# Optimization experiments

Hardware: AMD Instinct MI355X
Metric: run time of the kernel (lower is better)

## Reference

```python
import jax, jax.numpy as jnp
import numpy as np

H_Q, H_KV, D_HEAD = 32, 4, 128

def setup_inputs() -> dict:
    key = jax.random.key(0)
    ks = jax.random.split(key, 5)
    B, S, H = 1, 4096, 2048
    hidden_states = jax.random.normal(ks[0], (B, S, H), jnp.float32)
    Wq = jax.random.normal(ks[1], (H, H_Q * D_HEAD), jnp.float32) * 0.02
    Wk = jax.random.normal(ks[2], (H, H_KV * D_HEAD), jnp.float32) * 0.02
    Wv = jax.random.normal(ks[3], (H, H_KV * D_HEAD), jnp.float32) * 0.02
    Wo = jax.random.normal(ks[4], (H_Q * D_HEAD, H), jnp.float32) * 0.02
    position_ids = jnp.arange(S, dtype=jnp.int32)
    # causal boolean mask, used as-is by the layer when rank != 2
    attention_mask = jnp.tril(jnp.ones((S, S), dtype=bool))[None, None]
    return dict(hidden_states=hidden_states, Wq=Wq, Wk=Wk, Wv=Wv, Wo=Wo,
                position_ids=position_ids, attention_mask=attention_mask)

def _rope(x, positions):
    # x: [B, S, H, D]; rotate-half style RoPE, max_wavelength=10000, scaling=1
    d = x.shape[-1]
    inv_freq = 1.0 / (10000.0 ** (jnp.arange(0, d, 2, dtype=jnp.float32) / d))  # [d/2]
    freq = positions.astype(jnp.float32)[:, None] * inv_freq[None, :]           # [S, d/2]
    emb = jnp.concatenate([freq, freq], axis=-1)                                # [S, d]
    cos = jnp.cos(emb)[None, :, None, :]
    sin = jnp.sin(emb)[None, :, None, :]
    x1, x2 = jnp.split(x, 2, axis=-1)
    rot = jnp.concatenate([-x2, x1], axis=-1)
    return x * cos + rot * sin

def reference(hidden_states, Wq, Wk, Wv, Wo, position_ids, attention_mask):
    B, S, H = hidden_states.shape
    q = (hidden_states @ Wq).reshape(B, S, H_Q, D_HEAD)
    k = (hidden_states @ Wk).reshape(B, S, H_KV, D_HEAD)
    v = (hidden_states @ Wv).reshape(B, S, H_KV, D_HEAD)
    q = _rope(q, position_ids)
    k = _rope(k, position_ids)
    q = q.transpose(0, 2, 1, 3)                                   # [B,Hq,S,D]
    num_groups = H_Q // H_KV
    k = jnp.repeat(k.transpose(0, 2, 1, 3), num_groups, axis=1)   # [B,Hq,S,D]
    v = jnp.repeat(v.transpose(0, 2, 1, 3), num_groups, axis=1)
    scores = jnp.einsum('bhqd,bhkd->bhqk', q, k) / jnp.sqrt(jnp.float32(D_HEAD))
    scores = jnp.where(attention_mask, scores, jnp.float32(-1e9))
    weights = jax.nn.softmax(scores, axis=-1)
    out = jnp.einsum('bhqk,bhkd->bhqd', weights, v)
    out = out.transpose(0, 2, 1, 3).reshape(B, S, H_Q * D_HEAD)
    return out @ Wo
```

## Files before the change

kernel.cpp:

```cpp
#include <hip/hip_runtime.h>
#include <hip/hip_bf16.h>

typedef __attribute__((ext_vector_type(8))) short bf16x8;
typedef __attribute__((ext_vector_type(4))) float f32x4;
typedef __attribute__((ext_vector_type(16))) float f32x16;

#define WAIT_VMCNT(n) asm volatile("s_waitcnt vmcnt(" #n ")" ::: "memory")
#define WAIT_LGKM0()  asm volatile("s_waitcnt lgkmcnt(0)" ::: "memory")

__device__ __forceinline__ unsigned short f2b(float f) {
  __hip_bfloat16 h = __float2bfloat16(f);
  return __builtin_bit_cast(unsigned short, h);
}
__device__ __forceinline__ float b2f(unsigned short u) {
  return __bfloat162float(__builtin_bit_cast(__hip_bfloat16, u));
}
__device__ __forceinline__ unsigned int pk2(float a, float b) {
  unsigned int r;
  asm("v_cvt_pk_bf16_f32 %0, %1, %2" : "=v"(r) : "v"(a), "v"(b));
  return r;
}

__device__ __forceinline__ void gld_lds16(const void* g, void* l) {
  __builtin_amdgcn_global_load_lds(
      (const __attribute__((address_space(1))) unsigned int*)g,
      (__attribute__((address_space(3))) unsigned int*)l, 16, 0, 0);
}

__global__ void convert_kernel(const float* __restrict__ in, unsigned short* __restrict__ out, int n4) {
  int i = blockIdx.x * blockDim.x + threadIdx.x;
  if (i >= n4) return;
  float4 v = ((const float4*)in)[i];
  uint2 o;
  o.x = pk2(v.x, v.y);
  o.y = pk2(v.z, v.w);
  *(uint2*)(out + (size_t)i * 4) = o;
}

__global__ void transpose_convert_kernel(const float* __restrict__ in, unsigned short* __restrict__ out,
                                         int R, int C) {
  __shared__ float tile[32][33];
  int c0 = blockIdx.x * 32, r0 = blockIdx.y * 32;
  int tx = threadIdx.x, ty = threadIdx.y;
#pragma unroll
  for (int k = 0; k < 32; k += 8)
    tile[ty + k][tx] = in[(size_t)(r0 + ty + k) * C + (c0 + tx)];
  __syncthreads();
#pragma unroll
  for (int k = 0; k < 32; k += 8)
    out[(size_t)(c0 + ty + k) * R + (r0 + tx)] = f2b(tile[tx][ty + k]);
}

__global__ void rope_kernel(unsigned short* __restrict__ buf, const int* __restrict__ pos,
                            int log2h, int rowstride, float outscale, int total) {
  int idx = blockIdx.x * blockDim.x + threadIdx.x;
  if (idx >= total) return;
  int i = idx & 63;
  int h = (idx >> 6) & ((1 << log2h) - 1);
  int s = idx >> (6 + log2h);
  float inv = expf(-0.14391156831212787f * (float)i);
  float f = (float)pos[s] * inv;
  float sn, cs;
  sincosf(f, &sn, &cs);
  unsigned short* p = buf + (size_t)s * rowstride + (h << 7) + i;
  float x1 = b2f(p[0]);
  float x2 = b2f(p[64]);
  p[0]  = f2b((x1 * cs - x2 * sn) * outscale);
  p[64] = f2b((x2 * cs + x1 * sn) * outscale);
}

template <int OUT_MODE, int BN>
__global__ __launch_bounds__(512, 2) void gemm256_kernel(const unsigned short* __restrict__ A,
                                                         const unsigned short* __restrict__ Bt,
                                                         void* __restrict__ Cv,
                                                         void* __restrict__ C1,
                                                         void* __restrict__ C2,
                                                         int M, int N, int K) {
  constexpr int WN = BN / 4;
  constexpr int NI = WN / 16;
  constexpr int B_IT = BN * 8 / 512;
  __shared__ unsigned short As[2][256 * 64];
  __shared__ unsigned short Bs[2][BN * 64];

  int tid = threadIdx.x, lane = tid & 63, wave = tid >> 6;
  int wm = wave >> 2, wn = wave & 3;

  int gx = gridDim.x, nwg = gx * gridDim.y;
  int lin = blockIdx.y * gx + blockIdx.x;
  int swz = (lin & 7) * (nwg >> 3) + (lin >> 3);
  int m0 = (swz / gx) * 256, n0 = (swz % gx) * BN;

  int row0 = tid >> 3, ch = tid & 7;
  const unsigned short* pa0 = A + (size_t)(m0 + row0) * K + ((ch ^ (row0 & 7)) << 3);
  const unsigned short* pb0 = Bt + (size_t)(n0 + row0) * K + ((ch ^ (row0 & 7)) << 3);
  size_t rstep = (size_t)64 * K;

  auto stage = [&](int b, int kt) {
    const unsigned short* a = pa0 + (size_t)kt * 64;
    const unsigned short* bb = pb0 + (size_t)kt * 64;
#pragma unroll
    for (int it = 0; it < 4; ++it)
      gld_lds16(a + it * rstep, (unsigned short*)As[b] + (it * 512 + tid) * 8);
#pragma unroll
    for (int it = 0; it < B_IT; ++it)
      gld_lds16(bb + it * rstep, (unsigned short*)Bs[b] + (it * 512 + tid) * 8);
  };

  f32x4 acc[8][NI] = {};

  int nk = K >> 6;
  stage(0, 0);
  stage(1, 1);
  for (int kt = 0; kt < nk; ++kt) {
    int cur = kt & 1;
    if (kt + 1 < nk) {
      if constexpr (BN == 256) WAIT_VMCNT(8); else WAIT_VMCNT(6);
    } else {
      WAIT_VMCNT(0);
    }
    __builtin_amdgcn_s_barrier();

    bf16x8 af[8][2], bfr[NI][2];
#pragma unroll
    for (int mi = 0; mi < 8; ++mi) {
      int r = wm * 128 + mi * 16 + (lane & 15);
#pragma unroll
      for (int kk = 0; kk < 2; ++kk)
        af[mi][kk] = *(const bf16x8*)((const char*)As[cur] +
                      r * 128 + (((kk * 4 + (lane >> 4)) ^ (r & 7)) << 4));
    }
#pragma unroll
    for (int ni = 0; ni < NI; ++ni) {
      int r = wn * WN + ni * 16 + (lane & 15);
#pragma unroll
      for (int kk = 0; kk < 2; ++kk)
        bfr[ni][kk] = *(const bf16x8*)((const char*)Bs[cur] +
                       r * 128 + (((kk * 4 + (lane >> 4)) ^ (r & 7)) << 4));
    }
    WAIT_LGKM0();
    __builtin_amdgcn_s_barrier();
    if (kt + 2 < nk) stage(cur, kt + 2);

    __builtin_amdgcn_s_setprio(1);
#pragma unroll
    for (int mi = 0; mi < 8; ++mi)
#pragma unroll
      for (int ni = 0; ni < NI; ++ni)
#pragma unroll
        for (int kk = 0; kk < 2; ++kk)
          acc[mi][ni] = __builtin_amdgcn_mfma_f32_16x16x32_bf16(af[mi][kk], bfr[ni][kk],
                                                                acc[mi][ni], 0, 0, 0);
    __builtin_amdgcn_s_setprio(0);
  }

#pragma unroll
  for (int mi = 0; mi < 8; ++mi) {
#pragma unroll
    for (int ni = 0; ni < NI; ++ni) {
      int col = n0 + wn * WN + ni * 16 + (lane & 15);
      int rbase = m0 + wm * 128 + mi * 16 + (lane >> 4) * 4;
      if (OUT_MODE == 1) {
#pragma unroll
        for (int j = 0; j < 4; ++j)
          ((float*)Cv)[(size_t)(rbase + j) * N + col] = acc[mi][ni][j];
      } else {
        if (col < 4096) {
#pragma unroll
          for (int j = 0; j < 4; ++j)
            ((unsigned short*)Cv)[(size_t)(rbase + j) * 4096 + col] = f2b(acc[mi][ni][j]);
        } else if (col < 4608) {
          int c2 = col - 4096;
#pragma unroll
          for (int j = 0; j < 4; ++j)
            ((unsigned short*)C1)[(size_t)(rbase + j) * 512 + c2] = f2b(acc[mi][ni][j]);
        } else {
          int cv = col - 4608;
          int hk = cv >> 7, d = cv & 127;
          uint2 u;
          u.x = pk2(acc[mi][ni][0], acc[mi][ni][1]);
          u.y = pk2(acc[mi][ni][2], acc[mi][ni][3]);
          size_t addr = (size_t)hk * 524288 + (size_t)(rbase >> 6) * 8192 + d * 64 + (rbase & 63);
          *(uint2*)((unsigned short*)C2 + addr) = u;
        }
      }
    }
  }
}

__global__ __launch_bounds__(512) void attn_kernel(const unsigned short* __restrict__ Q,
                                                   const unsigned short* __restrict__ Kp,
                                                   const unsigned short* __restrict__ Vt,
                                                   unsigned short* __restrict__ O) {
  __shared__ unsigned short k_lds[3][64 * 128];
  __shared__ unsigned short vt_lds[3][128 * 64];

  int lin = blockIdx.y * 8 + blockIdx.x;
  int h = (lin & 7) * 4 + (lin >> 6);
  int xpair = (lin >> 3) & 7;
  int hk = h >> 3;
  int tid = threadIdx.x, lane = tid & 63, wave = tid >> 6;
  int l31 = lane & 31, hi = lane >> 5;

  int krow0 = tid >> 4, kch = tid & 15;
  int krow1 = krow0 + 32;
  const unsigned short* kp0 = Kp + (hk << 7) + (size_t)krow0 * 512 + ((kch ^ (krow0 & 15)) << 3);
  const unsigned short* kp1 = Kp + (hk << 7) + (size_t)krow1 * 512 + ((kch ^ (krow1 & 15)) << 3);
  int vd0 = tid >> 3, vsc = tid & 7;
  int vd1 = vd0 + 64;
  const unsigned short* vp0 = Vt + (size_t)hk * 524288 + vd0 * 64 + ((vsc ^ (vd0 & 7)) << 3);
  const unsigned short* vp1 = Vt + (size_t)hk * 524288 + vd1 * 64 + ((vsc ^ (vd1 & 7)) << 3);

  auto stage_tile = [&](int b, int t) {
    gld_lds16(kp0 + (size_t)t * 32768, (unsigned short*)k_lds[b] + tid * 8);
    gld_lds16(kp1 + (size_t)t * 32768, (unsigned short*)k_lds[b] + (512 + tid) * 8);
    gld_lds16(vp0 + (size_t)t * 8192, (unsigned short*)vt_lds[b] + tid * 8);
    gld_lds16(vp1 + (size_t)t * 8192, (unsigned short*)vt_lds[b] + (512 + tid) * 8);
  };

  for (int pass = 0; pass < 2; ++pass) {
    int SB = pass ? (15 - xpair) : xpair;
    int qt = SB * 8 + wave;
    int qrow = qt * 32 + l31;
    int tdiag = qt >> 1;
    int ntiles = 4 * SB + 4;

    bf16x8 qf[8];
#pragma unroll
    for (int kk = 0; kk < 8; ++kk)
      qf[kk] = *(const bf16x8*)(Q + (size_t)qrow * 4096 + (h << 7) + kk * 16 + hi * 8);

    f32x16 o_acc[4] = {};
    float m_run = -3.0e38f, l_run = 0.0f;

    __syncthreads();
    stage_tile(0, 0);
    stage_tile(1, 1);
    int cur = 0;
    for (int t0 = 0; t0 < ntiles; ++t0) {
      if (t0 + 1 < ntiles) WAIT_VMCNT(4); else WAIT_VMCNT(0);
      __builtin_amdgcn_s_barrier();
      if (t0 + 2 < ntiles) {
        int b2 = cur + 2; if (b2 >= 3) b2 -= 3;
        stage_tile(b2, t0 + 2);
      }

      if (t0 <= tdiag) {
        int s0 = t0 * 64;
        f32x16 sacc[2] = {};
        __builtin_amdgcn_s_setprio(1);
#pragma unroll
        for (int kk = 0; kk < 8; ++kk) {
#pragma unroll
          for (int t = 0; t < 2; ++t) {
            bf16x8 kf = *(const bf16x8*)((const char*)k_lds[cur] +
                         ((t * 32 + l31) * 256 + (((kk * 2 + hi) ^ (l31 & 15)) << 4)));
            sacc[t] = __builtin_amdgcn_mfma_f32_32x32x16_bf16(kf, qf[kk], sacc[t], 0, 0, 0);
          }
        }
        __builtin_amdgcn_s_setprio(0);

        float mx = -3.0e38f;
        if (t0 == tdiag) {
#pragma unroll
          for (int t = 0; t < 2; ++t)
#pragma unroll
            for (int r = 0; r < 16; ++r) {
              int sg = s0 + t * 32 + (r & 3) + 8 * (r >> 2) + 4 * hi;
              float v = sacc[t][r];
              v = (sg <= qrow) ? v : -3.0e38f;
              sacc[t][r] = v;
              mx = fmaxf(mx, v);
            }
        } else {
#pragma unroll
          for (int t = 0; t < 2; ++t)
#pragma unroll
            for (int r = 0; r < 16; ++r)
              mx = fmaxf(mx, sacc[t][r]);
        }
        mx = fmaxf(mx, __shfl_xor(mx, 32));
        if (!__all(mx <= m_run + 11.5416f)) {
          float m_new = fmaxf(m_run, mx);
          float corr = exp2f(m_run - m_new);
          l_run *= corr;
#pragma unroll
          for (int ds = 0; ds < 4; ++ds)
#pragma unroll
            for (int r = 0; r < 16; ++r) o_acc[ds][r] *= corr;
          m_run = m_new;
        }
        float rsum = 0.0f;
#pragma unroll
        for (int t = 0; t < 2; ++t)
#pragma unroll
          for (int r = 0; r < 16; ++r) {
            float e = exp2f(sacc[t][r] - m_run);
            sacc[t][r] = e;
            rsum += e;
          }
        l_run += rsum + __shfl_xor(rsum, 32);

        bf16x8 pb[4];
#pragma unroll
        for (int kk = 0; kk < 4; ++kk) {
          int t = kk >> 1;
          int b0 = (kk & 1) * 8;
          unsigned int a0 = pk2(sacc[t][b0 + 0], sacc[t][b0 + 1]);
          unsigned int a1 = pk2(sacc[t][b0 + 2], sacc[t][b0 + 3]);
          unsigned int c0 = pk2(sacc[t][b0 + 4], sacc[t][b0 + 5]);
          unsigned int c1 = pk2(sacc[t][b0 + 6], sacc[t][b0 + 7]);
          unsigned int snd0 = hi ? a0 : c0, snd1 = hi ? a1 : c1;
          unsigned int rcv0 = __shfl_xor(snd0, 32);
          unsigned int rcv1 = __shfl_xor(snd1, 32);
          unsigned int own0 = hi ? c0 : a0, own1 = hi ? c1 : a1;
          uint4 w;
          w.x = hi ? rcv0 : own0;
          w.y = hi ? rcv1 : own1;
          w.z = hi ? own0 : rcv0;
          w.w = hi ? own1 : rcv1;
          pb[kk] = __builtin_bit_cast(bf16x8, w);
        }

        __builtin_amdgcn_s_setprio(1);
#pragma unroll
        for (int ds = 0; ds < 4; ++ds) {
#pragma unroll
          for (int kk = 0; kk < 4; ++kk) {
            bf16x8 vf = *(const bf16x8*)((const char*)vt_lds[cur] +
                         ((ds * 32 + l31) * 128 + (((kk * 2 + hi) ^ (l31 & 7)) << 4)));
            o_acc[ds] = __builtin_amdgcn_mfma_f32_32x32x16_bf16(vf, pb[kk], o_acc[ds], 0, 0, 0);
          }
        }
        __builtin_amdgcn_s_setprio(0);
      }
      cur = (cur == 2) ? 0 : cur + 1;
    }

    __syncthreads();

    float inv_l = 1.0f / l_run;
    char* scr = (char*)k_lds + wave * 2304;
#pragma unroll
    for (int ds = 0; ds < 4; ++ds) {
#pragma unroll
      for (int rp = 0; rp < 8; ++rp) {
        int r = rp * 2;
        int d_loc = (r & 3) + 8 * (r >> 2) + 4 * hi;
        *(unsigned int*)(scr + l31 * 72 + ((d_loc >> 1) << 2)) =
            pk2(o_acc[ds][r] * inv_l, o_acc[ds][r + 1] * inv_l);
      }
      uint2 u0 = *(uint2*)(scr + l31 * 72 + hi * 32 + 0);
      uint2 u1 = *(uint2*)(scr + l31 * 72 + hi * 32 + 8);
      uint2 u2 = *(uint2*)(scr + l31 * 72 + hi * 32 + 16);
      uint2 u3 = *(uint2*)(scr + l31 * 72 + hi * 32 + 24);
      unsigned short* op = O + (size_t)qrow * 4096 + (h << 7) + ds * 32 + hi * 16;
      uint4 s0v; s0v.x = u0.x; s0v.y = u0.y; s0v.z = u1.x; s0v.w = u1.y;
      uint4 s1v; s1v.x = u2.x; s1v.y = u2.y; s1v.z = u3.x; s1v.w = u3.y;
      *(uint4*)(op) = s0v;
      *(uint4*)(op + 8) = s1v;
    }
  }
}

extern "C" void kernel_launch(void* const* d_in, const int* in_sizes, int n_in,
                              void* d_out, int out_size, void* d_ws, size_t ws_size,
                              hipStream_t stream) {
  const float* X  = (const float*)d_in[0];
  const float* Wq = (const float*)d_in[1];
  const float* Wk = (const float*)d_in[2];
  const float* Wv = (const float*)d_in[3];
  const float* Wo = (const float*)d_in[4];
  const int* pos  = (const int*)d_in[5];

  const size_t MB = 1u << 20;
  char* w = (char*)d_ws;
  unsigned short* Xb  = (unsigned short*)(w + 0 * MB);
  unsigned short* Wqt = (unsigned short*)(w + 16 * MB);
  unsigned short* Wkt = (unsigned short*)(w + 32 * MB);
  unsigned short* Wvt = (unsigned short*)(w + 34 * MB);
  unsigned short* Wot = (unsigned short*)(w + 36 * MB);
  unsigned short* Qb  = (unsigned short*)(w + 52 * MB);
  unsigned short* Kb  = (unsigned short*)(w + 84 * MB);
  unsigned short* Vtb = (unsigned short*)(w + 88 * MB);
  unsigned short* Ob  = (unsigned short*)(w + 92 * MB);

  convert_kernel<<<8192, 256, 0, stream>>>(X, Xb, 4096 * 2048 / 4);
  transpose_convert_kernel<<<dim3(128, 64), dim3(32, 8), 0, stream>>>(Wq, Wqt, 2048, 4096);
  transpose_convert_kernel<<<dim3(16, 64),  dim3(32, 8), 0, stream>>>(Wk, Wkt, 2048, 512);
  transpose_convert_kernel<<<dim3(16, 64),  dim3(32, 8), 0, stream>>>(Wv, Wvt, 2048, 512);
  transpose_convert_kernel<<<dim3(64, 128), dim3(32, 8), 0, stream>>>(Wo, Wot, 4096, 2048);

  gemm256_kernel<3, 256><<<dim3(20, 16), 512, 0, stream>>>(Xb, Wqt, Qb, Kb, Vtb, 4096, 5120, 2048);

  rope_kernel<<<(4096 * 32 * 64) / 256, 256, 0, stream>>>(Qb, pos, 5, 4096, 0.12752792534390558f, 4096 * 32 * 64);
  rope_kernel<<<(4096 * 4 * 64) / 256,  256, 0, stream>>>(Kb, pos, 2, 512, 1.0f, 4096 * 4 * 64);

  attn_kernel<<<dim3(8, 32), 512, 0, stream>>>(Qb, Kb, Vtb, Ob);

  gemm256_kernel<1, 128><<<dim3(16, 16), 512, 0, stream>>>(Ob, Wot, d_out, nullptr, nullptr, 4096, 2048, 4096);
}
```

Measured before the change: 437.2 us.

## Split fused QKV GEMM into Q GEMM and separate KV GEMM; prefetch V fragments

Replaces the single 4096x5120 QKV projection GEMM (320 blocks of 256x256) with a 256-block Q GEMM and a separate 128x128-tile K/V GEMM, so each launch's grid lines up with the number of compute units instead of leaving a partial wave. In the attention kernel it also loads all V fragments from LDS before the softmax, so the LDS reads overlap the softmax arithmetic. The costs are an extra kernel launch, the X matrix being read twice, and higher register pressure in the attention kernel. The KV kernel relies on Wkt and Wvt sitting contiguously in the workspace so they form one 1024-row B matrix, and its LDS tiles are not swizzled, which may cause bank conflicts.

```diff
diff --git a/kernel.cpp b/kernel.cpp
--- a/kernel.cpp
+++ b/kernel.cpp
@@ -73,8 +73,6 @@
 __global__ __launch_bounds__(512, 2) void gemm256_kernel(const unsigned short* __restrict__ A,
                                                          const unsigned short* __restrict__ Bt,
                                                          void* __restrict__ Cv,
-                                                         void* __restrict__ C1,
-                                                         void* __restrict__ C2,
                                                          int M, int N, int K) {
   constexpr int WN = BN / 4;
   constexpr int NI = WN / 16;
@@ -159,29 +157,98 @@
     for (int ni = 0; ni < NI; ++ni) {
       int col = n0 + wn * WN + ni * 16 + (lane & 15);
       int rbase = m0 + wm * 128 + mi * 16 + (lane >> 4) * 4;
-      if (OUT_MODE == 1) {
+#pragma unroll
+      for (int j = 0; j < 4; ++j) {
+        if (OUT_MODE == 1)
+          ((float*)Cv)[(size_t)(rbase + j) * N + col] = acc[mi][ni][j];
+        else
+          ((unsigned short*)Cv)[(size_t)(rbase + j) * N + col] = f2b(acc[mi][ni][j]);
+      }
+    }
+  }
+}
+
+__global__ __launch_bounds__(256) void gemm_kv_kernel(const unsigned short* __restrict__ A,
+                                                      const unsigned short* __restrict__ Bt,
+                                                      unsigned short* __restrict__ Kb,
+                                                      unsigned short* __restrict__ Vt,
+                                                      int K) {
+  __shared__ unsigned short As[3][128 * 32];
+  __shared__ unsigned short Bs[3][128 * 32];
+  int tid = threadIdx.x;
+  int lane = tid & 63;
+  int wave = tid >> 6;
+
+  int nwg = gridDim.x * gridDim.y;
+  int lin = blockIdx.y * gridDim.x + blockIdx.x;
+  int cpx = nwg >> 3;
+  int swz = (lin & 7) * cpx + (lin >> 3);
+  int m0 = (swz / gridDim.x) * 128, n0 = (swz % gridDim.x) * 128;
+
+  int wr = wave >> 1, wc = wave & 1;
+  f32x4 acc[4][4] = {};
+
+  int row0 = tid >> 2, cc0 = tid & 3;
+  const unsigned short* pa0 = A + (size_t)(m0 + row0) * K + cc0 * 8;
+  const unsigned short* pa1 = A + (size_t)(m0 + row0 + 64) * K + cc0 * 8;
+  const unsigned short* pb0 = Bt + (size_t)(n0 + row0) * K + cc0 * 8;
+  const unsigned short* pb1 = Bt + (size_t)(n0 + row0 + 64) * K + cc0 * 8;
+
+  auto stage = [&](int b, int k0) {
+    gld_lds16(pa0 + k0, (unsigned short*)As[b] + tid * 8);
+    gld_lds16(pa1 + k0, (unsigned short*)As[b] + (256 + tid) * 8);
+    gld_lds16(pb0 + k0, (unsigned short*)Bs[b] + tid * 8);
+    gld_lds16(pb1 + k0, (unsigned short*)Bs[b] + (256 + tid) * 8);
+  };
+
+  int nk = K >> 5;
+  stage(0, 0);
+  stage(1, 32);
+  int cur = 0;
+  for (int ki = 0; ki < nk; ++ki) {
+    if (ki + 1 < nk) WAIT_VMCNT(4); else WAIT_VMCNT(0);
+    __builtin_amdgcn_s_barrier();
+    if (ki + 2 < nk) {
+      int b2 = cur + 2; if (b2 >= 3) b2 -= 3;
+      stage(b2, (ki + 2) * 32);
+    }
+    bf16x8 af[4], bfr[4];
+#pragma unroll
+    for (int mi = 0; mi < 4; ++mi) {
+      int r = wr * 64 + mi * 16 + (lane & 15);
+      af[mi] = *(const bf16x8*)((const char*)As[cur] + r * 64 + (lane >> 4) * 16);
+    }
+#pragma unroll
+    for (int ni = 0; ni < 4; ++ni) {
+      int r = wc * 64 + ni * 16 + (lane & 15);
+      bfr[ni] = *(const bf16x8*)((const char*)Bs[cur] + r * 64 + (lane >> 4) * 16);
+    }
+#pragma unroll
+    for (int mi = 0; mi < 4; ++mi)
+#pragma unroll
+      for (int ni = 0; ni < 4; ++ni)
+        acc[mi][ni] = __builtin_amdgcn_mfma_f32_16x16x32_bf16(af[mi], bfr[ni], acc[mi][ni], 0, 0, 0);
+    cur = (cur == 2) ? 0 : cur + 1;
+  }
+
+#pragma unroll
+  for (int mi = 0; mi < 4; ++mi) {
+#pragma unroll
+    for (int ni = 0; ni < 4; ++ni) {
+      int col = n0 + wc * 64 + ni * 16 + (lane & 15);
+      int rbase = m0 + wr * 64 + mi * 16 + (lane >> 4) * 4;
+      if (col < 512) {
 #pragma unroll
         for (int j = 0; j < 4; ++j)
-          ((float*)Cv)[(size_t)(rbase + j) * N + col] = acc[mi][ni][j];
+          Kb[(size_t)(rbase + j) * 512 + col] = f2b(acc[mi][ni][j]);
       } else {
-        if (col < 4096) {
-#pragma unroll
-          for (int j = 0; j < 4; ++j)
-            ((unsigned short*)Cv)[(size_t)(rbase + j) * 4096 + col] = f2b(acc[mi][ni][j]);
-        } else if (col < 4608) {
-          int c2 = col - 4096;
-#pragma unroll
-          for (int j = 0; j < 4; ++j)
-            ((unsigned short*)C1)[(size_t)(rbase + j) * 512 + c2] = f2b(acc[mi][ni][j]);
-        } else {
-          int cv = col - 4608;
-          int hk = cv >> 7, d = cv & 127;
-          uint2 u;
-          u.x = pk2(acc[mi][ni][0], acc[mi][ni][1]);
-          u.y = pk2(acc[mi][ni][2], acc[mi][ni][3]);
-          size_t addr = (size_t)hk * 524288 + (size_t)(rbase >> 6) * 8192 + d * 64 + (rbase & 63);
-          *(uint2*)((unsigned short*)C2 + addr) = u;
-        }
+        int cv = col - 512;
+        int hk = cv >> 7, d = cv & 127;
+        uint2 u;
+        u.x = pk2(acc[mi][ni][0], acc[mi][ni][1]);
+        u.y = pk2(acc[mi][ni][2], acc[mi][ni][3]);
+        size_t addr = (size_t)hk * 524288 + (size_t)(rbase >> 6) * 8192 + d * 64 + (rbase & 63);
+        *(uint2*)(Vt + addr) = u;
       }
     }
   }
@@ -258,6 +325,14 @@
           }
         }
         __builtin_amdgcn_s_setprio(0);
+
+        bf16x8 vfr[4][4];
+#pragma unroll
+        for (int ds = 0; ds < 4; ++ds)
+#pragma unroll
+          for (int kk = 0; kk < 4; ++kk)
+            vfr[ds][kk] = *(const bf16x8*)((const char*)vt_lds[cur] +
+                           ((ds * 32 + l31) * 128 + (((kk * 2 + hi) ^ (l31 & 7)) << 4)));
 
         float mx = -3.0e38f;
         if (t0 == tdiag) {
@@ -323,14 +398,10 @@
 
         __builtin_amdgcn_s_setprio(1);
 #pragma unroll
-        for (int ds = 0; ds < 4; ++ds) {
-#pragma unroll
-          for (int kk = 0; kk < 4; ++kk) {
-            bf16x8 vf = *(const bf16x8*)((const char*)vt_lds[cur] +
-                         ((ds * 32 + l31) * 128 + (((kk * 2 + hi) ^ (l31 & 7)) << 4)));
-            o_acc[ds] = __builtin_amdgcn_mfma_f32_32x32x16_bf16(vf, pb[kk], o_acc[ds], 0, 0, 0);
-          }
-        }
+        for (int ds = 0; ds < 4; ++ds)
+#pragma unroll
+          for (int kk = 0; kk < 4; ++kk)
+            o_acc[ds] = __builtin_amdgcn_mfma_f32_32x32x16_bf16(vfr[ds][kk], pb[kk], o_acc[ds], 0, 0, 0);
         __builtin_amdgcn_s_setprio(0);
       }
       cur = (cur == 2) ? 0 : cur + 1;
@@ -390,12 +461,13 @@
   transpose_convert_kernel<<<dim3(16, 64),  dim3(32, 8), 0, stream>>>(Wv, Wvt, 2048, 512);
   transpose_convert_kernel<<<dim3(64, 128), dim3(32, 8), 0, stream>>>(Wo, Wot, 4096, 2048);
 
-  gemm256_kernel<3, 256><<<dim3(20, 16), 512, 0, stream>>>(Xb, Wqt, Qb, Kb, Vtb, 4096, 5120, 2048);
+  gemm256_kernel<0, 256><<<dim3(16, 16), 512, 0, stream>>>(Xb, Wqt, Qb, 4096, 4096, 2048);
+  gemm_kv_kernel<<<dim3(8, 32), 256, 0, stream>>>(Xb, Wkt, Kb, Vtb, 2048);
 
   rope_kernel<<<(4096 * 32 * 64) / 256, 256, 0, stream>>>(Qb, pos, 5, 4096, 0.12752792534390558f, 4096 * 32 * 64);
   rope_kernel<<<(4096 * 4 * 64) / 256,  256, 0, stream>>>(Kb, pos, 2, 512, 1.0f, 4096 * 4 * 64);
 
   attn_kernel<<<dim3(8, 32), 512, 0, stream>>>(Qb, Kb, Vtb, Ob);
 
-  gemm256_kernel<1, 128><<<dim3(16, 16), 512, 0, stream>>>(Ob, Wot, d_out, nullptr, nullptr, 4096, 2048, 4096);
-}
+  gemm256_kernel<1, 128><<<dim3(16, 16), 512, 0, stream>>>(Ob, Wot, d_out, 4096, 2048, 4096);
+}
```

Result: no change. 435.6 us (-0.4%).
